# Performance work log

Measured on AMD Instinct MI355X. Metric: run time of the kernel, lower is better.

Reference implementation:

```python
import jax, jax.numpy as jnp
import numpy as np

B, S = 2, 2048          # packed prefill: 2 sequences of 2048 tokens
T = B * S
HID = 3584
H, KV, D = 16, 8, 256   # query heads, kv heads, head_dim (num_groups = 2)
SCALE = 256.0 ** -0.5   # query_pre_attn_scalar ** -0.5
SOFTCAP = 50.0
WINDOW = 1024           # sliding_window (window_size_left)
ROPE_THETA = 10000.0


def _rope_cos_sin():
    # TGI PositionRotaryEmbedding: per-token cos/sin of shape [T, D//2]
    inv_freq = 1.0 / (ROPE_THETA ** (np.arange(0, D, 2, dtype=np.float32) / D))
    pos = np.tile(np.arange(S, dtype=np.float32), B)  # positions restart per sequence
    freqs = pos[:, None] * inv_freq[None, :]          # [T, D/2]
    return jnp.asarray(np.cos(freqs)), jnp.asarray(np.sin(freqs))


def _apply_rope(x, cos, sin):
    # neox-style rotate-half; x: [T, h, D], cos/sin: [T, D/2]
    x1, x2 = x[..., : D // 2], x[..., D // 2 :]
    c, s = cos[:, None, :], sin[:, None, :]
    return jnp.concatenate([x1 * c - x2 * s, x2 * c + x1 * s], axis=-1)


def setup_inputs() -> dict:
    key = jax.random.key(0)
    k1, k2, k3 = jax.random.split(key, 3)
    cos, sin = _rope_cos_sin()
    return {
        "hidden_states": jax.random.normal(k1, (T, HID), dtype=jnp.float32),
        "cos": cos,
        "sin": sin,
        "w_qkv": jax.random.normal(k2, ((H + 2 * KV) * D, HID), dtype=jnp.float32) * 0.02,
        "w_o": jax.random.normal(k3, (HID, H * D), dtype=jnp.float32) * 0.02,
    }


def reference(hidden_states, cos, sin, w_qkv, w_o):
    qkv = hidden_states @ w_qkv.T                      # [T, (H+2KV)*D]
    q = qkv[:, : H * D].reshape(T, H, D)
    k = qkv[:, H * D : (H + KV) * D].reshape(T, KV, D)
    v = qkv[:, (H + KV) * D :].reshape(T, KV, D)

    q = _apply_rope(q, cos, sin)
    k = _apply_rope(k, cos, sin)

    # unpack varlen batch (equal-length sequences)
    q = q.reshape(B, S, H, D)
    # GQA: repeat each kv head num_groups=2 times (kv_head_mapping)
    k = jnp.repeat(k.reshape(B, S, KV, D), H // KV, axis=2)
    v = jnp.repeat(v.reshape(B, S, KV, D), H // KV, axis=2)

    scores = jnp.einsum("bqhd,bkhd->bhqk", q, k) * SCALE
    scores = SOFTCAP * jnp.tanh(scores / SOFTCAP)      # logit softcapping

    i = jnp.arange(S)[:, None]
    j = jnp.arange(S)[None, :]
    allowed = (j <= i) & (j >= i - WINDOW)             # causal + sliding window left
    scores = jnp.where(allowed[None, None], scores, jnp.finfo(scores.dtype).min)

    probs = jax.nn.softmax(scores, axis=-1)
    out = jnp.einsum("bhqk,bkhd->bqhd", probs, v)      # [B, S, H, D]
    return out.reshape(T, H * D) @ w_o.T               # [T, HID]
```

## Files before the change

### kernel.cpp

```cpp
#include <hip/hip_runtime.h>

typedef __bf16 bf16x8 __attribute__((ext_vector_type(8)));
typedef __bf16 bf16x4 __attribute__((ext_vector_type(4)));
typedef float  f32x4  __attribute__((ext_vector_type(4)));

#define AS1 __attribute__((address_space(1)))
#define AS3 __attribute__((address_space(3)))

__device__ __forceinline__ void async16(const void* g, void* l) {
  __builtin_amdgcn_global_load_lds((const AS1 void*)g, (AS3 void*)l, 16, 0, 0);
}

static constexpr int T_   = 4096;
static constexpr int Sq   = 2048;
static constexpr int HID  = 3584;
static constexpr int NH   = 16;
static constexpr int NKV  = 8;
static constexpr int DH   = 256;
static constexpr float SCALE_   = 0.0625f;
static constexpr float SOFTCAP_ = 50.0f;
static constexpr int WINDOW_    = 1024;

__global__ __launch_bounds__(256) void cast_f32_bf16(const float4* __restrict__ in,
                                                     bf16x4* __restrict__ out, int n4) {
  int i = blockIdx.x * 256 + threadIdx.x;
  int stride = gridDim.x * 256;
  for (; i < n4; i += stride) {
    float4 v = in[i];
    bf16x4 o;
    o[0] = (__bf16)v.x; o[1] = (__bf16)v.y; o[2] = (__bf16)v.z; o[3] = (__bf16)v.w;
    out[i] = o;
  }
}

template <bool OUT_BF16>
__global__ __launch_bounds__(256) void gemm_bt(const __bf16* __restrict__ A,
                                               const __bf16* __restrict__ B,
                                               __bf16* __restrict__ Cb,
                                               float* __restrict__ Cf,
                                               int M, int N, int K) {
  __shared__ __bf16 lA[128 * 64];
  __shared__ __bf16 lB[128 * 64];
  const int tid  = threadIdx.x;
  const int w    = tid >> 6;
  const int lane = tid & 63;
  const int mrow = lane & 15;
  const int quad = lane >> 4;
  const int sw   = mrow & 7;
  const int tileN = blockIdx.x * 128;
  const int tileM = blockIdx.y * 128;
  const int wr = (w >> 1) * 64;
  const int wc = (w & 1) * 64;

  f32x4 acc[4][4];
#pragma unroll
  for (int i = 0; i < 4; ++i)
#pragma unroll
    for (int j = 0; j < 4; ++j) acc[i][j] = (f32x4){0.f, 0.f, 0.f, 0.f};

  const int rsub = tid >> 3;
  const int usw  = (tid & 7) ^ (rsub & 7);
  const int ccol = usw * 8;

  for (int k0 = 0; k0 < K; k0 += 64) {
#pragma unroll
    for (int it = 0; it < 4; ++it) {
      int row = it * 32 + rsub;
      const __bf16* ga = A + (size_t)(tileM + row) * K + k0 + ccol;
      const __bf16* gb = B + (size_t)(tileN + row) * K + k0 + ccol;
      async16(ga, &lA[(it * 256 + w * 64) * 8]);
      async16(gb, &lB[(it * 256 + w * 64) * 8]);
    }
    __syncthreads();
#pragma unroll
    for (int kk = 0; kk < 2; ++kk) {
      bf16x8 af[4], bfr[4];
#pragma unroll
      for (int i = 0; i < 4; ++i)
        af[i] = *(const bf16x8*)&lA[(wr + i * 16 + mrow) * 64 + (((kk * 4 + quad) ^ sw) * 8)];
#pragma unroll
      for (int j = 0; j < 4; ++j)
        bfr[j] = *(const bf16x8*)&lB[(wc + j * 16 + mrow) * 64 + (((kk * 4 + quad) ^ sw) * 8)];
#pragma unroll
      for (int i = 0; i < 4; ++i)
#pragma unroll
        for (int j = 0; j < 4; ++j)
          acc[i][j] = __builtin_amdgcn_mfma_f32_16x16x32_bf16(af[i], bfr[j], acc[i][j], 0, 0, 0);
    }
    __syncthreads();
  }

#pragma unroll
  for (int i = 0; i < 4; ++i) {
    int row0 = tileM + wr + i * 16 + quad * 4;
#pragma unroll
    for (int j = 0; j < 4; ++j) {
      int col = tileN + wc + j * 16 + mrow;
#pragma unroll
      for (int r = 0; r < 4; ++r) {
        if constexpr (OUT_BF16)
          Cb[(size_t)(row0 + r) * N + col] = (__bf16)acc[i][j][r];
        else
          Cf[(size_t)(row0 + r) * N + col] = acc[i][j][r];
      }
    }
  }
}

__global__ __launch_bounds__(256) void rope_relayout(const __bf16* __restrict__ qkv,
                                                     const float* __restrict__ cosb,
                                                     const float* __restrict__ sinb,
                                                     __bf16* __restrict__ qout,
                                                     __bf16* __restrict__ kout) {
  const int t = blockIdx.x;
  const int b = t >> 11, s = t & (Sq - 1);
  const int d = threadIdx.x & 127;
  const int half = threadIdx.x >> 7;
  const float c  = cosb[t * 128 + d];
  const float sn = sinb[t * 128 + d];
  const size_t base = (size_t)t * 8192;
#pragma unroll
  for (int it = 0; it < 12; ++it) {
    int seg = it * 2 + half;
    float x1 = (float)qkv[base + seg * 256 + d];
    float x2 = (float)qkv[base + seg * 256 + 128 + d];
    float o1 = x1 * c - x2 * sn;
    float o2 = x2 * c + x1 * sn;
    if (seg < 16) {
      size_t o = ((size_t)(b * NH + seg) * Sq + s) * DH + d;
      qout[o] = (__bf16)o1;
      qout[o + 128] = (__bf16)o2;
    } else {
      int kvh = seg - 16;
      size_t o = ((size_t)(b * NKV + kvh) * Sq + s) * DH + d;
      kout[o] = (__bf16)o1;
      kout[o + 128] = (__bf16)o2;
    }
  }
}

__global__ __launch_bounds__(256) void vtrans(const __bf16* __restrict__ qkv,
                                              __bf16* __restrict__ vt) {
  __shared__ __bf16 tile[64][72];
  const int bkv = blockIdx.y;
  const int b = bkv >> 3, kv = bkv & 7;
  const int st0 = (blockIdx.x >> 2) * 64;
  const int dt0 = (blockIdx.x & 3) * 64;
  const int tid = threadIdx.x;
#pragma unroll
  for (int it = 0; it < 2; ++it) {
    int g = it * 256 + tid;
    int r = g >> 3, cc = (g & 7) * 8;
    const __bf16* src = qkv + (size_t)(b * Sq + st0 + r) * 8192 + 6144 + kv * 256 + dt0 + cc;
    bf16x8 v = *(const bf16x8*)src;
#pragma unroll
    for (int j = 0; j < 8; ++j) tile[r][cc + j] = v[j];
  }
  __syncthreads();
#pragma unroll
  for (int it = 0; it < 2; ++it) {
    int g = it * 256 + tid;
    int r = g >> 3, cc = (g & 7) * 8;
    bf16x8 v;
#pragma unroll
    for (int j = 0; j < 8; ++j) v[j] = tile[cc + j][r];
    *(bf16x8*)(vt + ((size_t)bkv * DH + dt0 + r) * Sq + st0 + cc) = v;
  }
}

template <int MODE>
__device__ __forceinline__ void softcap_tile(const f32x4 sc[4], float lrun[4],
                                             __bf16* Pl, int pbase, int mrow,
                                             int kt, int qi) {
#pragma unroll
  for (int j = 0; j < 4; ++j) {
    const int kj = kt + j * 16 + mrow;
#pragma unroll
    for (int r = 0; r < 4; ++r) {
      float z = sc[j][r] * (SCALE_ / SOFTCAP_);
      float z2 = z * z;
      float u = __builtin_fmaf(z2, 0.13333333f, -0.33333333f);
      float th = z * __builtin_fmaf(z2, u, 1.0f);
      float pe = __builtin_fmaf(th, 72.134752f, -72.134752f);
      if (MODE == 1) pe = (kj <= qi + r) ? pe : -1000.0f;
      if (MODE == 2) pe = (kj >= qi + r - WINDOW_) ? pe : -1000.0f;
      float p = __builtin_amdgcn_exp2f(pe);
      lrun[r] += p;
      Pl[pbase + r * 72 + j * 16 + mrow] = (__bf16)p;
    }
  }
}

__global__ __launch_bounds__(256, 3) void attn_kernel(const __bf16* __restrict__ q,
                                                      const __bf16* __restrict__ k,
                                                      const __bf16* __restrict__ vt,
                                                      __bf16* __restrict__ out) {
  __shared__ __bf16 Kl[64 * 256];
  __shared__ __bf16 Vl[128 * 64];
  __bf16* Pl  = Kl;
  __bf16* V1l = Kl + 8192;

  const int bid0 = blockIdx.x;
  const int gidx = (bid0 & 7) * 128 + (bid0 >> 3);
  const int grp  = gidx >> 5;
  const int qt   = 31 - (gidx & 31);
  const int h    = grp & 15;
  const int b    = grp >> 4;
  const int kvh  = h >> 1;
  const int q0   = qt * 64;
  const int tid = threadIdx.x, w = tid >> 6, lane = tid & 63;
  const int mrow = lane & 15, quad = lane >> 4;
  const int sw = mrow & 7;

  bf16x8 qf[8];
  const __bf16* qbase = q + ((size_t)(b * NH + h) * Sq + q0 + w * 16 + mrow) * DH;
#pragma unroll
  for (int kf = 0; kf < 8; ++kf) qf[kf] = *(const bf16x8*)(qbase + kf * 32 + quad * 8);

  f32x4 o[16];
#pragma unroll
  for (int n = 0; n < 16; ++n) o[n] = (f32x4){0.f, 0.f, 0.f, 0.f};
  float lrun[4] = {0.f, 0.f, 0.f, 0.f};

  int kt_lo = q0 - WINDOW_; if (kt_lo < 0) kt_lo = 0;
  const __bf16* kbase = k + (size_t)(b * NKV + kvh) * Sq * DH;
  const __bf16* vbase = vt + (size_t)(b * NKV + kvh) * DH * Sq;
  const int qi = q0 + w * 16 + quad * 4;
  const int pbase = w * 1152 + quad * 4 * 72;

  for (int kt = kt_lo; kt <= q0; kt += 64) {
#pragma unroll
    for (int it = 0; it < 8; ++it) {
      int g = it * 256 + tid;
      int rk = g >> 5, uk = g & 31;
      const __bf16* gk = kbase + (size_t)(kt + rk) * DH + (uk ^ (rk & 7)) * 8;
      async16(gk, &Kl[(it * 256 + w * 64) * 8]);
    }
#pragma unroll
    for (int it = 0; it < 4; ++it) {
      int g = it * 256 + tid;
      int rv = g >> 3, uv = g & 7;
      const __bf16* gv = vbase + (size_t)rv * Sq + kt + (uv ^ (rv & 7)) * 8;
      async16(gv, &Vl[(it * 256 + w * 64) * 8]);
    }
    __syncthreads();

    f32x4 sc[4];
#pragma unroll
    for (int j = 0; j < 4; ++j) sc[j] = (f32x4){0.f, 0.f, 0.f, 0.f};
#pragma unroll
    for (int kf = 0; kf < 8; ++kf)
#pragma unroll
      for (int j = 0; j < 4; ++j) {
        bf16x8 kfr = *(const bf16x8*)&Kl[(j * 16 + mrow) * 256 + ((kf * 4 + quad) ^ sw) * 8];
        sc[j] = __builtin_amdgcn_mfma_f32_16x16x32_bf16(qf[kf], kfr, sc[j], 0, 0, 0);
      }
    __syncthreads();

#pragma unroll
    for (int it = 0; it < 4; ++it) {
      int g = it * 256 + tid;
      int rv = g >> 3, uv = g & 7;
      const __bf16* gv = vbase + (size_t)(128 + rv) * Sq + kt + (uv ^ (rv & 7)) * 8;
      async16(gv, &V1l[(it * 256 + w * 64) * 8]);
    }

    if (kt == q0)                 softcap_tile<1>(sc, lrun, Pl, pbase, mrow, kt, qi);
    else if (kt == q0 - WINDOW_)  softcap_tile<2>(sc, lrun, Pl, pbase, mrow, kt, qi);
    else                          softcap_tile<0>(sc, lrun, Pl, pbase, mrow, kt, qi);

    bf16x8 pf0 = *(const bf16x8*)&Pl[w * 1152 + mrow * 72 + 0 * 32 + quad * 8];
    bf16x8 pf1 = *(const bf16x8*)&Pl[w * 1152 + mrow * 72 + 1 * 32 + quad * 8];

#pragma unroll
    for (int kk = 0; kk < 2; ++kk) {
      bf16x8 pf = kk ? pf1 : pf0;
#pragma unroll
      for (int n = 0; n < 8; ++n) {
        bf16x8 vf = *(const bf16x8*)&Vl[(n * 16 + mrow) * 64 + ((kk * 4 + quad) ^ sw) * 8];
        o[n] = __builtin_amdgcn_mfma_f32_16x16x32_bf16(pf, vf, o[n], 0, 0, 0);
      }
    }
    __syncthreads();
#pragma unroll
    for (int kk = 0; kk < 2; ++kk) {
      bf16x8 pf = kk ? pf1 : pf0;
#pragma unroll
      for (int n = 8; n < 16; ++n) {
        bf16x8 vf = *(const bf16x8*)&V1l[((n - 8) * 16 + mrow) * 64 + ((kk * 4 + quad) ^ sw) * 8];
        o[n] = __builtin_amdgcn_mfma_f32_16x16x32_bf16(pf, vf, o[n], 0, 0, 0);
      }
    }
    __syncthreads();
  }

#pragma unroll
  for (int m = 1; m < 16; m <<= 1)
#pragma unroll
    for (int r = 0; r < 4; ++r) lrun[r] += __shfl_xor(lrun[r], m, 64);

  float inv[4];
#pragma unroll
  for (int r = 0; r < 4; ++r) inv[r] = 1.f / lrun[r];
  const size_t trow = (size_t)(b * Sq + q0 + w * 16 + quad * 4);
#pragma unroll
  for (int n = 0; n < 16; ++n)
#pragma unroll
    for (int r = 0; r < 4; ++r)
      out[(trow + r) * 4096 + h * DH + n * 16 + mrow] = (__bf16)(o[n][r] * inv[r]);
}

extern "C" void kernel_launch(void* const* d_in, const int* in_sizes, int n_in,
                              void* d_out, int out_size, void* d_ws, size_t ws_size,
                              hipStream_t stream) {
  (void)in_sizes; (void)n_in; (void)out_size; (void)ws_size;
  const float* hs   = (const float*)d_in[0];
  const float* cosb = (const float*)d_in[1];
  const float* sinb = (const float*)d_in[2];
  const float* wqkv = (const float*)d_in[3];
  const float* wo   = (const float*)d_in[4];
  float* out = (float*)d_out;
  char* ws = (char*)d_ws;

  __bf16* hs_bf   = (__bf16*)(ws + 0);
  __bf16* wo_bf   = (__bf16*)(ws + 0);
  __bf16* wqkv_bf = (__bf16*)(ws + 29360128);
  __bf16* attn_bf = (__bf16*)(ws + 29360128);
  __bf16* qkv_bf  = (__bf16*)(ws + 88080384);
  __bf16* q_bf    = (__bf16*)(ws + 155189248);
  __bf16* k_bf    = (__bf16*)(ws + 188743680);
  __bf16* vt_bf   = (__bf16*)(ws + 205520896);

  cast_f32_bf16<<<1024, 256, 0, stream>>>((const float4*)hs, (bf16x4*)hs_bf, T_ * HID / 4);
  cast_f32_bf16<<<1024, 256, 0, stream>>>((const float4*)wqkv, (bf16x4*)wqkv_bf, 8192 * HID / 4);

  gemm_bt<true><<<dim3(8192 / 128, T_ / 128), 256, 0, stream>>>(
      hs_bf, wqkv_bf, qkv_bf, nullptr, T_, 8192, HID);

  rope_relayout<<<T_, 256, 0, stream>>>(qkv_bf, cosb, sinb, q_bf, k_bf);

  vtrans<<<dim3(128, 16), 256, 0, stream>>>(qkv_bf, vt_bf);

  cast_f32_bf16<<<1024, 256, 0, stream>>>((const float4*)wo, (bf16x4*)wo_bf, HID * 4096 / 4);

  attn_kernel<<<dim3(2 * NH * (Sq / 64)), 256, 0, stream>>>(q_bf, k_bf, vt_bf, attn_bf);

  gemm_bt<false><<<dim3(HID / 128, T_ / 128), 256, 0, stream>>>(
      attn_bf, wo_bf, nullptr, out, T_, HID, 4096);
}
```

Measured before the change: 817.7 us.

## Merge cast and aux kernels, load full V tile once in attention

Both input casts now run in a single launch, and RoPE relayout, V transpose and the w_o cast are merged into one block-partitioned kernel, cutting launch count and letting independent work overlap. The attention kernel gets dedicated LDS for the full 256-wide V tile and for P, so V loads are issued together with K and one barrier per iteration goes away. This raises LDS use per block, and launch bounds drop from 3 to 2 blocks per CU, so occupancy falls.

```diff
diff --git a/kernel.cpp b/kernel.cpp
--- a/kernel.cpp
+++ b/kernel.cpp
@@ -21,15 +21,18 @@
 static constexpr float SOFTCAP_ = 50.0f;
 static constexpr int WINDOW_    = 1024;
 
-__global__ __launch_bounds__(256) void cast_f32_bf16(const float4* __restrict__ in,
-                                                     bf16x4* __restrict__ out, int n4) {
+__global__ __launch_bounds__(256) void cast2_f32_bf16(const float4* __restrict__ a,
+                                                      bf16x4* __restrict__ oa, int n4a,
+                                                      const float4* __restrict__ b,
+                                                      bf16x4* __restrict__ ob, int n4b) {
   int i = blockIdx.x * 256 + threadIdx.x;
   int stride = gridDim.x * 256;
-  for (; i < n4; i += stride) {
-    float4 v = in[i];
+  int ntot = n4a + n4b;
+  for (; i < ntot; i += stride) {
+    const float4 v = (i < n4a) ? a[i] : b[i - n4a];
     bf16x4 o;
     o[0] = (__bf16)v.x; o[1] = (__bf16)v.y; o[2] = (__bf16)v.z; o[3] = (__bf16)v.w;
-    out[i] = o;
+    if (i < n4a) oa[i] = o; else ob[i - n4a] = o;
   }
 }
 
@@ -107,64 +110,80 @@
   }
 }
 
-__global__ __launch_bounds__(256) void rope_relayout(const __bf16* __restrict__ qkv,
-                                                     const float* __restrict__ cosb,
-                                                     const float* __restrict__ sinb,
-                                                     __bf16* __restrict__ qout,
-                                                     __bf16* __restrict__ kout) {
-  const int t = blockIdx.x;
-  const int b = t >> 11, s = t & (Sq - 1);
-  const int d = threadIdx.x & 127;
-  const int half = threadIdx.x >> 7;
-  const float c  = cosb[t * 128 + d];
-  const float sn = sinb[t * 128 + d];
-  const size_t base = (size_t)t * 8192;
-#pragma unroll
-  for (int it = 0; it < 12; ++it) {
-    int seg = it * 2 + half;
-    float x1 = (float)qkv[base + seg * 256 + d];
-    float x2 = (float)qkv[base + seg * 256 + 128 + d];
-    float o1 = x1 * c - x2 * sn;
-    float o2 = x2 * c + x1 * sn;
-    if (seg < 16) {
-      size_t o = ((size_t)(b * NH + seg) * Sq + s) * DH + d;
-      qout[o] = (__bf16)o1;
-      qout[o + 128] = (__bf16)o2;
-    } else {
-      int kvh = seg - 16;
-      size_t o = ((size_t)(b * NKV + kvh) * Sq + s) * DH + d;
-      kout[o] = (__bf16)o1;
-      kout[o + 128] = (__bf16)o2;
-    }
-  }
-}
-
-__global__ __launch_bounds__(256) void vtrans(const __bf16* __restrict__ qkv,
-                                              __bf16* __restrict__ vt) {
+__global__ __launch_bounds__(256) void aux_fused(const __bf16* __restrict__ qkv,
+                                                 const float* __restrict__ cosb,
+                                                 const float* __restrict__ sinb,
+                                                 __bf16* __restrict__ qout,
+                                                 __bf16* __restrict__ kout,
+                                                 __bf16* __restrict__ vt,
+                                                 const float4* __restrict__ wo,
+                                                 bf16x4* __restrict__ wo_bf) {
   __shared__ __bf16 tile[64][72];
-  const int bkv = blockIdx.y;
-  const int b = bkv >> 3, kv = bkv & 7;
-  const int st0 = (blockIdx.x >> 2) * 64;
-  const int dt0 = (blockIdx.x & 3) * 64;
+  const int blk = blockIdx.x;
   const int tid = threadIdx.x;
-#pragma unroll
-  for (int it = 0; it < 2; ++it) {
-    int g = it * 256 + tid;
-    int r = g >> 3, cc = (g & 7) * 8;
-    const __bf16* src = qkv + (size_t)(b * Sq + st0 + r) * 8192 + 6144 + kv * 256 + dt0 + cc;
-    bf16x8 v = *(const bf16x8*)src;
-#pragma unroll
-    for (int j = 0; j < 8; ++j) tile[r][cc + j] = v[j];
-  }
-  __syncthreads();
-#pragma unroll
-  for (int it = 0; it < 2; ++it) {
-    int g = it * 256 + tid;
-    int r = g >> 3, cc = (g & 7) * 8;
-    bf16x8 v;
-#pragma unroll
-    for (int j = 0; j < 8; ++j) v[j] = tile[cc + j][r];
-    *(bf16x8*)(vt + ((size_t)bkv * DH + dt0 + r) * Sq + st0 + cc) = v;
+
+  if (blk < 4096) {
+    const int t = blk;
+    const int b = t >> 11, s = t & (Sq - 1);
+    const int d = tid & 127;
+    const int half = tid >> 7;
+    const float c  = cosb[t * 128 + d];
+    const float sn = sinb[t * 128 + d];
+    const size_t base = (size_t)t * 8192;
+#pragma unroll
+    for (int it = 0; it < 12; ++it) {
+      int seg = it * 2 + half;
+      float x1 = (float)qkv[base + seg * 256 + d];
+      float x2 = (float)qkv[base + seg * 256 + 128 + d];
+      float o1 = x1 * c - x2 * sn;
+      float o2 = x2 * c + x1 * sn;
+      if (seg < 16) {
+        size_t o = ((size_t)(b * NH + seg) * Sq + s) * DH + d;
+        qout[o] = (__bf16)o1;
+        qout[o + 128] = (__bf16)o2;
+      } else {
+        int kvh = seg - 16;
+        size_t o = ((size_t)(b * NKV + kvh) * Sq + s) * DH + d;
+        kout[o] = (__bf16)o1;
+        kout[o + 128] = (__bf16)o2;
+      }
+    }
+  } else if (blk < 6144) {
+    const int flat = blk - 4096;
+    const int bx  = flat & 127;
+    const int bkv = flat >> 7;
+    const int b = bkv >> 3, kv = bkv & 7;
+    const int st0 = (bx >> 2) * 64;
+    const int dt0 = (bx & 3) * 64;
+#pragma unroll
+    for (int it = 0; it < 2; ++it) {
+      int g = it * 256 + tid;
+      int r = g >> 3, cc = (g & 7) * 8;
+      const __bf16* src = qkv + (size_t)(b * Sq + st0 + r) * 8192 + 6144 + kv * 256 + dt0 + cc;
+      bf16x8 v = *(const bf16x8*)src;
+#pragma unroll
+      for (int j = 0; j < 8; ++j) tile[r][cc + j] = v[j];
+    }
+    __syncthreads();
+#pragma unroll
+    for (int it = 0; it < 2; ++it) {
+      int g = it * 256 + tid;
+      int r = g >> 3, cc = (g & 7) * 8;
+      bf16x8 v;
+#pragma unroll
+      for (int j = 0; j < 8; ++j) v[j] = tile[cc + j][r];
+      *(bf16x8*)(vt + ((size_t)bkv * DH + dt0 + r) * Sq + st0 + cc) = v;
+    }
+  } else {
+    const int n4 = HID * 4096 / 4;
+    int i = (blk - 6144) * 256 + tid;
+    const int stride = 1024 * 256;
+    for (; i < n4; i += stride) {
+      float4 v = wo[i];
+      bf16x4 o;
+      o[0] = (__bf16)v.x; o[1] = (__bf16)v.y; o[2] = (__bf16)v.z; o[3] = (__bf16)v.w;
+      wo_bf[i] = o;
+    }
   }
 }
 
@@ -191,14 +210,13 @@
   }
 }
 
-__global__ __launch_bounds__(256, 3) void attn_kernel(const __bf16* __restrict__ q,
+__global__ __launch_bounds__(256, 2) void attn_kernel(const __bf16* __restrict__ q,
                                                       const __bf16* __restrict__ k,
                                                       const __bf16* __restrict__ vt,
                                                       __bf16* __restrict__ out) {
   __shared__ __bf16 Kl[64 * 256];
-  __shared__ __bf16 Vl[128 * 64];
-  __bf16* Pl  = Kl;
-  __bf16* V1l = Kl + 8192;
+  __shared__ __bf16 Vl[256 * 64];
+  __shared__ __bf16 Pl[4 * 1152];
 
   const int bid0 = blockIdx.x;
   const int gidx = (bid0 & 7) * 128 + (bid0 >> 3);
@@ -237,7 +255,7 @@
       async16(gk, &Kl[(it * 256 + w * 64) * 8]);
     }
 #pragma unroll
-    for (int it = 0; it < 4; ++it) {
+    for (int it = 0; it < 8; ++it) {
       int g = it * 256 + tid;
       int rv = g >> 3, uv = g & 7;
       const __bf16* gv = vbase + (size_t)rv * Sq + kt + (uv ^ (rv & 7)) * 8;
@@ -255,15 +273,6 @@
         bf16x8 kfr = *(const bf16x8*)&Kl[(j * 16 + mrow) * 256 + ((kf * 4 + quad) ^ sw) * 8];
         sc[j] = __builtin_amdgcn_mfma_f32_16x16x32_bf16(qf[kf], kfr, sc[j], 0, 0, 0);
       }
-    __syncthreads();
-
-#pragma unroll
-    for (int it = 0; it < 4; ++it) {
-      int g = it * 256 + tid;
-      int rv = g >> 3, uv = g & 7;
-      const __bf16* gv = vbase + (size_t)(128 + rv) * Sq + kt + (uv ^ (rv & 7)) * 8;
-      async16(gv, &V1l[(it * 256 + w * 64) * 8]);
-    }
 
     if (kt == q0)                 softcap_tile<1>(sc, lrun, Pl, pbase, mrow, kt, qi);
     else if (kt == q0 - WINDOW_)  softcap_tile<2>(sc, lrun, Pl, pbase, mrow, kt, qi);
@@ -276,18 +285,8 @@
     for (int kk = 0; kk < 2; ++kk) {
       bf16x8 pf = kk ? pf1 : pf0;
 #pragma unroll
-      for (int n = 0; n < 8; ++n) {
+      for (int n = 0; n < 16; ++n) {
         bf16x8 vf = *(const bf16x8*)&Vl[(n * 16 + mrow) * 64 + ((kk * 4 + quad) ^ sw) * 8];
-        o[n] = __builtin_amdgcn_mfma_f32_16x16x32_bf16(pf, vf, o[n], 0, 0, 0);
-      }
-    }
-    __syncthreads();
-#pragma unroll
-    for (int kk = 0; kk < 2; ++kk) {
-      bf16x8 pf = kk ? pf1 : pf0;
-#pragma unroll
-      for (int n = 8; n < 16; ++n) {
-        bf16x8 vf = *(const bf16x8*)&V1l[((n - 8) * 16 + mrow) * 64 + ((kk * 4 + quad) ^ sw) * 8];
         o[n] = __builtin_amdgcn_mfma_f32_16x16x32_bf16(pf, vf, o[n], 0, 0, 0);
       }
     }
@@ -331,17 +330,14 @@
   __bf16* k_bf    = (__bf16*)(ws + 188743680);
   __bf16* vt_bf   = (__bf16*)(ws + 205520896);
 
-  cast_f32_bf16<<<1024, 256, 0, stream>>>((const float4*)hs, (bf16x4*)hs_bf, T_ * HID / 4);
-  cast_f32_bf16<<<1024, 256, 0, stream>>>((const float4*)wqkv, (bf16x4*)wqkv_bf, 8192 * HID / 4);
+  cast2_f32_bf16<<<2048, 256, 0, stream>>>((const float4*)hs, (bf16x4*)hs_bf, T_ * HID / 4,
+                                           (const float4*)wqkv, (bf16x4*)wqkv_bf, 8192 * HID / 4);
 
   gemm_bt<true><<<dim3(8192 / 128, T_ / 128), 256, 0, stream>>>(
       hs_bf, wqkv_bf, qkv_bf, nullptr, T_, 8192, HID);
 
-  rope_relayout<<<T_, 256, 0, stream>>>(qkv_bf, cosb, sinb, q_bf, k_bf);
-
-  vtrans<<<dim3(128, 16), 256, 0, stream>>>(qkv_bf, vt_bf);
-
-  cast_f32_bf16<<<1024, 256, 0, stream>>>((const float4*)wo, (bf16x4*)wo_bf, HID * 4096 / 4);
+  aux_fused<<<7168, 256, 0, stream>>>(qkv_bf, cosb, sinb, q_bf, k_bf, vt_bf,
+                                      (const float4*)wo, (bf16x4*)wo_bf);
 
   attn_kernel<<<dim3(2 * NH * (Sq / 64)), 256, 0, stream>>>(q_bf, k_bf, vt_bf, attn_bf);
 
```

Result: faster. 780.3 us (-4.6%).
